# Optimization experiments

Measured on AMD Instinct MI355X. Metric: run time of the kernel, lower is better.

## Reference

```python
import jax, jax.numpy as jnp
import numpy as np

N = 4096        # num nodes
D = 512         # d_model (in_dim)
F = 512         # dff (out_dim)
H = 4           # num_heads
ALPHA = 0.3     # tf.keras LeakyReLU default


def setup_inputs() -> dict:
    key = jax.random.key(0)
    ks = jax.random.split(key, 9)
    s_in = 1.0 / np.sqrt(D)
    s_out = 1.0 / np.sqrt(F)
    return {
        "nodes": jax.random.normal(ks[0], (N, D), jnp.float32),
        "edges": jax.random.normal(ks[1], (N, D), jnp.float32),
        "labels": jax.random.normal(ks[2], (N, D), jnp.float32),
        # edge_layer Dense(dff)
        "We": jax.random.normal(ks[3], (D, F), jnp.float32) * s_in,
        "be": jnp.zeros((F,), jnp.float32),
        # per-head kernels stacked on leading head axis
        "W": jax.random.normal(ks[4], (H, D, F), jnp.float32) * s_in,
        "b": jax.random.normal(ks[5], (H, F), jnp.float32) * 0.01,
        "u": jax.random.normal(ks[6], (H, F), jnp.float32) * s_out,  # attn_kernel_self (squeezed)
        "v": jax.random.normal(ks[7], (H, F), jnp.float32) * s_out,  # attn_kernel_neighs (squeezed)
    }


def reference(nodes, edges, labels, We, be, W, b, u, v):
    # edge projection shared across heads: Dense(edges + labels)
    e = (edges + labels) @ We + be                       # [N, F]
    # per-head node projection: features = nodes @ W_h + b_h
    feats = jnp.einsum('nd,hdf->hnf', nodes, W) + b[:, None, :]   # [H, N, F]
    # rank-1 additive attention scores
    a_self = jnp.einsum('hnf,hf->hn', feats, u)          # [H, N]
    a_neigh = jnp.einsum('hnf,hf->hn', feats, v)         # [H, N]
    feats = feats + e[None]                              # [H, N, F]
    scores = a_self[:, :, None] * a_neigh[:, None, :]    # [H, N, N] outer product
    scores = jnp.where(scores >= 0, scores, ALPHA * scores)  # LeakyReLU(0.3)
    attn = jax.nn.softmax(scores, axis=-1)               # [H, N, N]
    out = jnp.einsum('hnm,hmf->hnf', attn, feats)        # [H, N, F]
    return jax.nn.relu(out.mean(axis=0))                 # [N, F]
```

## Files before the change

### kernel.cpp

```cpp
#include <hip/hip_runtime.h>

#define NN 4096
#define DD 512
#define FF 512
#define HH 4
#define KK 1024

typedef _Float16 f16;
typedef f16 f16x8 __attribute__((ext_vector_type(8)));
typedef f16 f16x4 __attribute__((ext_vector_type(4)));
typedef float f32x4 __attribute__((ext_vector_type(4)));

typedef __attribute__((address_space(1))) void gvoid;
typedef __attribute__((address_space(3))) void svoid;
__device__ __forceinline__ void glds16(const void* g, void* s) {
    __builtin_amdgcn_global_load_lds((gvoid*)g, (svoid*)s, 16, 0, 0);
}

__device__ __attribute__((aligned(16))) f16 g_catA[NN * KK];
__device__ __attribute__((aligned(16))) f16 g_catB[HH * FF * KK];
__device__ __attribute__((aligned(16))) f16 g_featsH[HH * FF * NN];
__device__ __attribute__((aligned(16))) f16 g_oaccH[(size_t)2 * HH * NN * FF];
__device__ float g_Zp[2 * HH * NN];
__device__ float g_bcat[HH * FF];
__device__ float g_tu[HH * DD], g_tv[HH * DD], g_bu[HH], g_bv[HH];
__device__ float g_p[HH * NN], g_q[HH * NN], g_M[HH * NN];

#define PREP_CONV 4104
#define PREP_TRAN 320
#define PREP_UV   513

__global__ __launch_bounds__(256) void k_prep(const float* __restrict__ nodes, const float* __restrict__ edges,
                                              const float* __restrict__ labels, const float* __restrict__ We,
                                              const float* __restrict__ W, const float* __restrict__ be,
                                              const float* __restrict__ b, const float* __restrict__ u,
                                              const float* __restrict__ v) {
    __shared__ float lds[64 * 65];
    int bx = blockIdx.x;
    int tid = threadIdx.x;
    if (bx < PREP_CONV) {
        int id = bx * 256 + tid;
        const int NQ = NN * DD / 4;
        if (id < NQ) {
            f32x4 vv = *(const f32x4*)(nodes + (size_t)id * 4);
            f16x4 ov;
#pragma unroll
            for (int k = 0; k < 4; ++k) ov[k] = (f16)vv[k];
            *(f16x4*)&g_catA[(size_t)(id >> 7) * KK + (id & 127) * 4] = ov;
            return;
        }
        id -= NQ;
        if (id < NQ) {
            f32x4 ev = *(const f32x4*)(edges  + (size_t)id * 4);
            f32x4 lv = *(const f32x4*)(labels + (size_t)id * 4);
            f16x4 ov;
#pragma unroll
            for (int k = 0; k < 4; ++k) ov[k] = (f16)(ev[k] + lv[k]);
            *(f16x4*)&g_catA[(size_t)(id >> 7) * KK + 512 + (id & 127) * 4] = ov;
            return;
        }
        id -= NQ;
        if (id < HH * FF) { g_bcat[id] = b[id] + be[id & 511]; return; }
        return;
    }
    if (bx < PREP_CONV + PREP_TRAN) {
        int bid = bx - PREP_CONV;
        int mi = bid >> 6;
        int t64 = bid & 63;
        const float* src = (mi == 0) ? We : (W + (size_t)(mi - 1) * DD * FF);
        int ti = t64 >> 3, tj = t64 & 7;
        int r = tid >> 2, cseg = (tid & 3) * 16;
#pragma unroll
        for (int kq = 0; kq < 4; ++kq) {
            f32x4 vv = *(const f32x4*)(src + (size_t)(ti * 64 + r) * 512 + tj * 64 + cseg + kq * 4);
            *(f32x4*)&lds[r * 65 + cseg + kq * 4] = vv;
        }
        __syncthreads();
        int fl = tid >> 2, dseg = (tid & 3) * 16;
        f16x8 o0, o1;
#pragma unroll
        for (int k = 0; k < 8; ++k) o0[k] = (f16)lds[(dseg + k) * 65 + fl];
#pragma unroll
        for (int k = 0; k < 8; ++k) o1[k] = (f16)lds[(dseg + 8 + k) * 65 + fl];
        size_t frow = (size_t)(tj * 64 + fl);
        size_t dcol = (size_t)(ti * 64 + dseg);
        if (mi == 0) {
#pragma unroll
            for (int hh = 0; hh < HH; ++hh) {
                size_t ob = ((size_t)hh * FF + frow) * KK + 512 + dcol;
                *(f16x8*)&g_catB[ob] = o0;
                *(f16x8*)&g_catB[ob + 8] = o1;
            }
        } else {
            size_t ob = ((size_t)(mi - 1) * FF + frow) * KK + dcol;
            *(f16x8*)&g_catB[ob] = o0;
            *(f16x8*)&g_catB[ob + 8] = o1;
        }
        return;
    }
    {
        int row = (bx - PREP_CONV - PREP_TRAN) * 4 + (tid >> 6);
        int lane = tid & 63;
        float su = 0.f, sv = 0.f;
        if (row < HH * DD) {
            int h = row >> 9, d = row & 511;
            size_t wb = (size_t)h * DD * FF + (size_t)d * FF;
#pragma unroll
            for (int j = 0; j < 8; ++j) {
                int f = lane + 64 * j;
                float wv = W[wb + f];
                su += wv * u[(size_t)h * FF + f];
                sv += wv * v[(size_t)h * FF + f];
            }
        } else if (row < HH * DD + HH) {
            int h = row - HH * DD;
#pragma unroll
            for (int j = 0; j < 8; ++j) {
                int f = lane + 64 * j;
                float bvv = b[(size_t)h * FF + f];
                su += bvv * u[(size_t)h * FF + f];
                sv += bvv * v[(size_t)h * FF + f];
            }
        }
#pragma unroll
        for (int m = 1; m < 64; m <<= 1) {
            su += __shfl_xor(su, m, 64);
            sv += __shfl_xor(sv, m, 64);
        }
        if (lane == 0 && row < HH * DD + HH) {
            if (row < HH * DD) { g_tu[row] = su; g_tv[row] = sv; }
            else { g_bu[row - HH * DD] = su; g_bv[row - HH * DD] = sv; }
        }
    }
}

__global__ __launch_bounds__(256) void k_pq() {
    int row = blockIdx.x * 4 + (threadIdx.x >> 6);
    int lane = threadIdx.x & 63;
    int h = row >> 12, n = row & 4095;
    const f16* nb = g_catA + (size_t)n * KK + lane * 8;
    const float* tu = g_tu + h * DD + lane * 8;
    const float* tv = g_tv + h * DD + lane * 8;
    f16x8 nv8 = *(const f16x8*)nb;
    f32x4 tu0 = *(const f32x4*)tu, tu1 = *(const f32x4*)(tu + 4);
    f32x4 tv0 = *(const f32x4*)tv, tv1 = *(const f32x4*)(tv + 4);
    float pa = 0.f, qa = 0.f;
#pragma unroll
    for (int j = 0; j < 4; ++j) {
        float nv = (float)nv8[j];
        pa += nv * tu0[j];
        qa += nv * tv0[j];
    }
#pragma unroll
    for (int j = 0; j < 4; ++j) {
        float nv = (float)nv8[4 + j];
        pa += nv * tu1[j];
        qa += nv * tv1[j];
    }
#pragma unroll
    for (int m = 1; m < 64; m <<= 1) {
        pa += __shfl_xor(pa, m, 64);
        qa += __shfl_xor(qa, m, 64);
    }
    if (lane == 0) {
        g_p[row] = pa + g_bu[h];
        g_q[row] = qa + g_bv[h];
    }
}

__global__ __launch_bounds__(256, 2) void k_gemm_feats() {
    __shared__ f16 As[128 * 128];
    __shared__ f16 Bs[128 * 128];
    int tid = threadIdx.x;
    int lane = tid & 63, wave = tid >> 6;
    int wr = wave & 1, wc = wave >> 1;
    int c = lane & 15, g = lane >> 4;
    int n0 = blockIdx.x * 128, f0 = blockIdx.y * 128;
    int h = blockIdx.z;
    const f16* Bgl = g_catB + (size_t)h * FF * KK;
    int r4 = lane >> 4;
    int ch = lane & 15;
    f32x4 acc[4][4] = {};
    for (int kk = 0; kk < KK; kk += 128) {
        __syncthreads();
#pragma unroll
        for (int j = 0; j < 8; ++j) {
            int rowb = wave * 32 + j * 4;
            int row = rowb + r4;
            int src = (ch ^ (row & 15)) * 8;
            glds16(g_catA + (size_t)(n0 + row) * KK + kk + src, &As[rowb * 128]);
            glds16(Bgl    + (size_t)(f0 + row) * KK + kk + src, &Bs[rowb * 128]);
        }
        __syncthreads();
#pragma unroll
        for (int s = 0; s < 4; ++s) {
            f16x8 af[4], bf[4];
#pragma unroll
            for (int i = 0; i < 4; ++i) {
                int ra = wr * 64 + i * 16 + c;
                af[i] = *(const f16x8*)&As[ra * 128 + (((s * 4 + g) ^ (ra & 15)) * 8)];
            }
#pragma unroll
            for (int jj = 0; jj < 4; ++jj) {
                int rb = wc * 64 + jj * 16 + c;
                bf[jj] = *(const f16x8*)&Bs[rb * 128 + (((s * 4 + g) ^ (rb & 15)) * 8)];
            }
#pragma unroll
            for (int i = 0; i < 4; ++i)
#pragma unroll
                for (int jj = 0; jj < 4; ++jj)
                    acc[i][jj] = __builtin_amdgcn_mfma_f32_16x16x32_f16(af[i], bf[jj], acc[i][jj], 0, 0, 0);
        }
    }
#pragma unroll
    for (int jj = 0; jj < 4; ++jj) {
        int f = f0 + wc * 64 + jj * 16 + c;
        float bv = g_bcat[h * FF + f];
#pragma unroll
        for (int i = 0; i < 4; ++i) {
            int r0 = n0 + wr * 64 + i * 16 + g * 4;
            f16x4 ov;
#pragma unroll
            for (int rr = 0; rr < 4; ++rr) ov[rr] = (f16)(acc[i][jj][rr] + bv);
            *(f16x4*)(g_featsH + ((size_t)h * FF + f) * NN + r0) = ov;
        }
    }
}

__global__ __launch_bounds__(256) void k_mstat() {
    __shared__ float red[256];
    int h = blockIdx.x;
    int tid = threadIdx.x;
    float lmax = -1e30f, lmin = 1e30f;
    for (int i = tid; i < NN; i += 256) {
        float qv = g_q[h * NN + i];
        lmax = fmaxf(lmax, qv);
        lmin = fminf(lmin, qv);
    }
    red[tid] = lmax;
    __syncthreads();
    for (int s = 128; s > 0; s >>= 1) {
        if (tid < s) red[tid] = fmaxf(red[tid], red[tid + s]);
        __syncthreads();
    }
    float qmax = red[0];
    __syncthreads();
    red[tid] = lmin;
    __syncthreads();
    for (int s = 128; s > 0; s >>= 1) {
        if (tid < s) red[tid] = fminf(red[tid], red[tid + s]);
        __syncthreads();
    }
    float qmin = red[0];
#pragma unroll
    for (int j = 0; j < 16; ++j) {
        int n = tid + j * 256;
        float pv = g_p[h * NN + n];
        float se = pv * (pv >= 0.f ? qmax : qmin);
        g_M[h * NN + n] = fmaxf(se, 0.3f * se);
    }
}

#define ALD 68
__global__ __launch_bounds__(512, 2) void k_gemm_out() {
    __shared__ f16 As[128 * ALD];
    __shared__ f16 BsL[512 * 32];
    __shared__ f16 BsH[512 * 32];
    int tid = threadIdx.x;
    int lane = tid & 63, wave = tid >> 6;
    int wr = wave & 1;
    int wf = wave >> 1;
    int c = lane & 15, g = lane >> 4;
    int n0 = blockIdx.x * 128;
    int h = blockIdx.y;
    int ks = blockIdx.z;
    int wn = tid >> 2, kq = (tid & 3) * 16;
    const float C = 0.015625f;
    float pv = g_p[h * NN + n0 + wn];
    float mv = g_M[h * NN + n0 + wn];
    const float* qh = g_q + h * NN + ks * 2048;
    const f16* Bgl = g_featsH + (size_t)h * FF * NN + (size_t)ks * 2048;
    int brow = lane >> 2;
    int bksw = ((lane & 3) ^ (brow & 3)) * 8;
    float zacc = 0.f;
    f32x4 acc[4][8] = {};
    for (int kk = 0; kk < 2048; kk += 64) {
        f16x8 w0, w1;
#pragma unroll
        for (int half = 0; half < 2; ++half) {
            f32x4 qa = *(const f32x4*)(qh + kk + kq + half * 8);
            f32x4 qb = *(const f32x4*)(qh + kk + kq + half * 8 + 4);
#pragma unroll
            for (int k = 0; k < 4; ++k) {
                float s = pv * qa[k];
                s = fmaxf(s, 0.3f * s);
                float e = __expf(s - mv) * C;
                zacc += e;
                if (half == 0) w0[k] = (f16)e;
                else           w1[k] = (f16)e;
            }
#pragma unroll
            for (int k = 0; k < 4; ++k) {
                float s = pv * qb[k];
                s = fmaxf(s, 0.3f * s);
                float e = __expf(s - mv) * C;
                zacc += e;
                if (half == 0) w0[4 + k] = (f16)e;
                else           w1[4 + k] = (f16)e;
            }
        }
        __syncthreads();
        *(f16x8*)&As[wn * ALD + kq] = w0;
        *(f16x8*)&As[wn * ALD + kq + 8] = w1;
#pragma unroll
        for (int j = 0; j < 4; ++j) {
            int frow = wave * 64 + j * 16;
            glds16(Bgl + (size_t)(frow + brow) * NN + kk + bksw,      &BsL[frow * 32]);
            glds16(Bgl + (size_t)(frow + brow) * NN + kk + 32 + bksw, &BsH[frow * 32]);
        }
        __syncthreads();
#pragma unroll
        for (int s = 0; s < 2; ++s) {
            const f16* Bsrc = (s == 0) ? BsL : BsH;
            f16x8 af[4], bfr[8];
#pragma unroll
            for (int i = 0; i < 4; ++i)
                af[i] = *(const f16x8*)&As[(wr * 64 + i * 16 + c) * ALD + s * 32 + g * 8];
#pragma unroll
            for (int jj = 0; jj < 8; ++jj)
                bfr[jj] = *(const f16x8*)&Bsrc[(wf * 128 + jj * 16 + c) * 32 + ((g ^ (c & 3)) * 8)];
#pragma unroll
            for (int i = 0; i < 4; ++i)
#pragma unroll
                for (int jj = 0; jj < 8; ++jj)
                    acc[i][jj] = __builtin_amdgcn_mfma_f32_16x16x32_f16(af[i], bfr[jj], acc[i][jj], 0, 0, 0);
        }
    }
    zacc += __shfl_xor(zacc, 1, 64);
    zacc += __shfl_xor(zacc, 2, 64);
    if ((tid & 3) == 0) g_Zp[(size_t)(h * 2 + ks) * NN + n0 + wn] = zacc;
    f16* O = g_oaccH + (size_t)(h * 2 + ks) * NN * FF;
#pragma unroll
    for (int jj = 0; jj < 8; ++jj) {
        int f = wf * 128 + jj * 16 + c;
#pragma unroll
        for (int i = 0; i < 4; ++i) {
            int r0 = n0 + wr * 64 + i * 16 + g * 4;
#pragma unroll
            for (int rr = 0; rr < 4; ++rr)
                O[(size_t)(r0 + rr) * FF + f] = (f16)acc[i][jj][rr];
        }
    }
}

__global__ void k_reduce(float* __restrict__ out) {
    int t = blockIdx.x * 256 + threadIdx.x;
    size_t i = (size_t)t * 4;
    int n = t >> 7;
    const size_t NF = (size_t)NN * FF;
    f32x4 s = {0.f, 0.f, 0.f, 0.f};
#pragma unroll
    for (int h = 0; h < HH; ++h) {
        float Z = g_Zp[(size_t)(2 * h) * NN + n] + g_Zp[(size_t)(2 * h + 1) * NN + n];
        float sc = 0.25f / Z;
        f16x4 a = *(const f16x4*)(g_oaccH + (size_t)(2 * h) * NF + i);
        f16x4 bsl = *(const f16x4*)(g_oaccH + (size_t)(2 * h + 1) * NF + i);
#pragma unroll
        for (int rr = 0; rr < 4; ++rr) s[rr] += ((float)a[rr] + (float)bsl[rr]) * sc;
    }
    f32x4 o;
#pragma unroll
    for (int rr = 0; rr < 4; ++rr) o[rr] = fmaxf(s[rr], 0.f);
    *(f32x4*)(out + i) = o;
}

extern "C" void kernel_launch(void* const* d_in, const int* in_sizes, int n_in,
                              void* d_out, int out_size, void* d_ws, size_t ws_size,
                              hipStream_t stream) {
    (void)in_sizes; (void)n_in; (void)out_size; (void)d_ws; (void)ws_size;
    const float* nodes  = (const float*)d_in[0];
    const float* edges  = (const float*)d_in[1];
    const float* labels = (const float*)d_in[2];
    const float* We     = (const float*)d_in[3];
    const float* be     = (const float*)d_in[4];
    const float* W      = (const float*)d_in[5];
    const float* b      = (const float*)d_in[6];
    const float* u      = (const float*)d_in[7];
    const float* v      = (const float*)d_in[8];

    k_prep<<<PREP_CONV + PREP_TRAN + PREP_UV, 256, 0, stream>>>(nodes, edges, labels, We, W, be, b, u, v);
    k_pq<<<4096, 256, 0, stream>>>();
    k_gemm_feats<<<dim3(32, 4, 4), 256, 0, stream>>>();
    k_mstat<<<HH, 256, 0, stream>>>();
    k_gemm_out<<<dim3(32, 4, 2), 512, 0, stream>>>();
    k_reduce<<<2048, 256, 0, stream>>>((float*)d_out);
}
```

Before: 243.7 us.

## Double-buffer LDS in output GEMM and overlap weight generation with MFMA

```diff
diff --git a/kernel.cpp b/kernel.cpp
--- a/kernel.cpp
+++ b/kernel.cpp
@@ -261,11 +261,28 @@
     }
 }
 
-#define ALD 68
+#define WCALC(qv, dstvec, idx)                                              \
+    {                                                                       \
+        float s_ = pv * (qv);                                               \
+        s_ = fmaxf(s_, 0.3f * s_);                                          \
+        float e_ = __builtin_amdgcn_exp2f(__builtin_fmaf(s_, L2E, -mvb));   \
+        zacc += e_;                                                         \
+        dstvec[idx] = (f16)e_;                                              \
+    }
+#define GEN16(q0, q1, q2, q3, w0, w1)                                       \
+    {                                                                       \
+        _Pragma("unroll") for (int k_ = 0; k_ < 4; ++k_) {                  \
+            WCALC((q0)[k_], w0, k_);                                        \
+            WCALC((q1)[k_], w0, 4 + k_);                                    \
+            WCALC((q2)[k_], w1, k_);                                        \
+            WCALC((q3)[k_], w1, 4 + k_);                                    \
+        }                                                                   \
+    }
+
 __global__ __launch_bounds__(512, 2) void k_gemm_out() {
-    __shared__ f16 As[128 * ALD];
-    __shared__ f16 BsL[512 * 32];
-    __shared__ f16 BsH[512 * 32];
+    __shared__ f16 As2[2][128 * 64];
+    __shared__ f16 BsL[2][512 * 32];
+    __shared__ f16 BsH[2][512 * 32];
     int tid = threadIdx.x;
     int lane = tid & 63, wave = tid >> 6;
     int wr = wave & 1;
@@ -275,66 +292,94 @@
     int h = blockIdx.y;
     int ks = blockIdx.z;
     int wn = tid >> 2, kq = (tid & 3) * 16;
-    const float C = 0.015625f;
+    const float L2E = 1.44269504f;
     float pv = g_p[h * NN + n0 + wn];
-    float mv = g_M[h * NN + n0 + wn];
+    float mvb = g_M[h * NN + n0 + wn] * L2E + 6.0f;
     const float* qh = g_q + h * NN + ks * 2048;
     const f16* Bgl = g_featsH + (size_t)h * FF * NN + (size_t)ks * 2048;
     int brow = lane >> 2;
     int bksw = ((lane & 3) ^ (brow & 3)) * 8;
+    int aw0 = wn * 64 + (((tid & 3) * 2 + 0) ^ (wn & 7)) * 8;
+    int aw1 = wn * 64 + (((tid & 3) * 2 + 1) ^ (wn & 7)) * 8;
     float zacc = 0.f;
     f32x4 acc[4][8] = {};
-    for (int kk = 0; kk < 2048; kk += 64) {
-        f16x8 w0, w1;
-#pragma unroll
-        for (int half = 0; half < 2; ++half) {
-            f32x4 qa = *(const f32x4*)(qh + kk + kq + half * 8);
-            f32x4 qb = *(const f32x4*)(qh + kk + kq + half * 8 + 4);
-#pragma unroll
-            for (int k = 0; k < 4; ++k) {
-                float s = pv * qa[k];
-                s = fmaxf(s, 0.3f * s);
-                float e = __expf(s - mv) * C;
-                zacc += e;
-                if (half == 0) w0[k] = (f16)e;
-                else           w1[k] = (f16)e;
-            }
-#pragma unroll
-            for (int k = 0; k < 4; ++k) {
-                float s = pv * qb[k];
-                s = fmaxf(s, 0.3f * s);
-                float e = __expf(s - mv) * C;
-                zacc += e;
-                if (half == 0) w0[4 + k] = (f16)e;
-                else           w1[4 + k] = (f16)e;
-            }
-        }
-        __syncthreads();
-        *(f16x8*)&As[wn * ALD + kq] = w0;
-        *(f16x8*)&As[wn * ALD + kq + 8] = w1;
+    f16x8 wA, wB;
+
+    {
+        const float* qp = qh + kq;
+        f32x4 q0 = *(const f32x4*)qp, q1 = *(const f32x4*)(qp + 4),
+              q2 = *(const f32x4*)(qp + 8), q3 = *(const f32x4*)(qp + 12);
+        GEN16(q0, q1, q2, q3, wA, wB);
+        *(f16x8*)&As2[0][aw0] = wA;
+        *(f16x8*)&As2[0][aw1] = wB;
 #pragma unroll
         for (int j = 0; j < 4; ++j) {
             int frow = wave * 64 + j * 16;
-            glds16(Bgl + (size_t)(frow + brow) * NN + kk + bksw,      &BsL[frow * 32]);
-            glds16(Bgl + (size_t)(frow + brow) * NN + kk + 32 + bksw, &BsH[frow * 32]);
-        }
-        __syncthreads();
-#pragma unroll
-        for (int s = 0; s < 2; ++s) {
-            const f16* Bsrc = (s == 0) ? BsL : BsH;
+            glds16(Bgl + (size_t)(frow + brow) * NN + bksw,      &BsL[0][frow * 32]);
+            glds16(Bgl + (size_t)(frow + brow) * NN + 32 + bksw, &BsH[0][frow * 32]);
+        }
+        const float* qp1 = qh + 64 + kq;
+        q0 = *(const f32x4*)qp1; q1 = *(const f32x4*)(qp1 + 4);
+        q2 = *(const f32x4*)(qp1 + 8); q3 = *(const f32x4*)(qp1 + 12);
+        GEN16(q0, q1, q2, q3, wA, wB);
+    }
+    __syncthreads();
+
+    int cur = 0;
+    for (int t = 0; t < 32; ++t) {
+        f32x4 q0, q1, q2, q3;
+        if (t < 30) {
+            const float* qp = qh + t * 64 + 128 + kq;
+            q0 = *(const f32x4*)qp; q1 = *(const f32x4*)(qp + 4);
+            q2 = *(const f32x4*)(qp + 8); q3 = *(const f32x4*)(qp + 12);
+        }
+        if (t < 31) {
+            int nxt = cur ^ 1;
+            int kk2 = t * 64 + 64;
+#pragma unroll
+            for (int j = 0; j < 4; ++j) {
+                int frow = wave * 64 + j * 16;
+                glds16(Bgl + (size_t)(frow + brow) * NN + kk2 + bksw,      &BsL[nxt][frow * 32]);
+                glds16(Bgl + (size_t)(frow + brow) * NN + kk2 + 32 + bksw, &BsH[nxt][frow * 32]);
+            }
+            *(f16x8*)&As2[nxt][aw0] = wA;
+            *(f16x8*)&As2[nxt][aw1] = wB;
+        }
+        {
             f16x8 af[4], bfr[8];
 #pragma unroll
-            for (int i = 0; i < 4; ++i)
-                af[i] = *(const f16x8*)&As[(wr * 64 + i * 16 + c) * ALD + s * 32 + g * 8];
+            for (int i = 0; i < 4; ++i) {
+                int ra = wr * 64 + i * 16 + c;
+                af[i] = *(const f16x8*)&As2[cur][ra * 64 + ((g ^ (ra & 7)) * 8)];
+            }
 #pragma unroll
             for (int jj = 0; jj < 8; ++jj)
-                bfr[jj] = *(const f16x8*)&Bsrc[(wf * 128 + jj * 16 + c) * 32 + ((g ^ (c & 3)) * 8)];
+                bfr[jj] = *(const f16x8*)&BsL[cur][(wf * 128 + jj * 16 + c) * 32 + ((g ^ (c & 3)) * 8)];
 #pragma unroll
             for (int i = 0; i < 4; ++i)
 #pragma unroll
                 for (int jj = 0; jj < 8; ++jj)
                     acc[i][jj] = __builtin_amdgcn_mfma_f32_16x16x32_f16(af[i], bfr[jj], acc[i][jj], 0, 0, 0);
         }
+        if (t < 30) GEN16(q0, q1, q2, q3, wA, wB);
+        {
+            f16x8 af[4], bfr[8];
+#pragma unroll
+            for (int i = 0; i < 4; ++i) {
+                int ra = wr * 64 + i * 16 + c;
+                af[i] = *(const f16x8*)&As2[cur][ra * 64 + (((4 + g) ^ (ra & 7)) * 8)];
+            }
+#pragma unroll
+            for (int jj = 0; jj < 8; ++jj)
+                bfr[jj] = *(const f16x8*)&BsH[cur][(wf * 128 + jj * 16 + c) * 32 + ((g ^ (c & 3)) * 8)];
+#pragma unroll
+            for (int i = 0; i < 4; ++i)
+#pragma unroll
+                for (int jj = 0; jj < 8; ++jj)
+                    acc[i][jj] = __builtin_amdgcn_mfma_f32_16x16x32_f16(af[i], bfr[jj], acc[i][jj], 0, 0, 0);
+        }
+        __syncthreads();
+        cur ^= 1;
     }
     zacc += __shfl_xor(zacc, 1, 64);
     zacc += __shfl_xor(zacc, 2, 64);
```

Measured after the change: 230.2 us. -5.5%, faster.
